# Kernel tuning notes

Measured on AMD Instinct MI355X. Metric: run time of the kernel, lower is better.

## Reference

```python
import jax, jax.numpy as jnp
import numpy as np
import math

D_MODEL = 1024
NUM_HEADS = 16
D_K = D_MODEL // NUM_HEADS


def setup_inputs() -> dict:
    key = jax.random.key(0)
    ks = jax.random.split(key, 9)
    s = 1.0 / math.sqrt(D_MODEL)
    x = jax.random.normal(ks[0], (2, 2048, D_MODEL), dtype=jnp.float32)
    # torch Linear params: weight [out, in], bias [out]
    Wq = jax.random.uniform(ks[1], (D_MODEL, D_MODEL), jnp.float32, -s, s)
    bq = jax.random.uniform(ks[2], (D_MODEL,), jnp.float32, -s, s)
    Wk = jax.random.uniform(ks[3], (D_MODEL, D_MODEL), jnp.float32, -s, s)
    bk = jax.random.uniform(ks[4], (D_MODEL,), jnp.float32, -s, s)
    Wv = jax.random.uniform(ks[5], (D_MODEL, D_MODEL), jnp.float32, -s, s)
    bv = jax.random.uniform(ks[6], (D_MODEL,), jnp.float32, -s, s)
    Wo = jax.random.uniform(ks[7], (D_MODEL, D_MODEL), jnp.float32, -s, s)
    bo = jax.random.uniform(ks[8], (D_MODEL,), jnp.float32, -s, s)
    return {"x": x, "Wq": Wq, "bq": bq, "Wk": Wk, "bk": bk,
            "Wv": Wv, "bv": bv, "Wo": Wo, "bo": bo}


def reference(x, Wq, bq, Wk, bk, Wv, bv, Wo, bo):
    B, T, _ = x.shape
    scale = 1.0 / math.sqrt(D_MODEL)  # NOTE: module scales by sqrt(d_model), not sqrt(d_k)

    def proj(W, b):
        # torch Linear: x @ W^T + b, then split heads -> [B, H, T, d_k]
        y = jnp.einsum('btd,ed->bte', x, W) + b
        return y.reshape(B, T, NUM_HEADS, D_K).transpose(0, 2, 1, 3)

    Q = proj(Wq, bq)
    K = proj(Wk, bk)
    V = proj(Wv, bv)
    logits = jnp.einsum('bhtd,bhsd->bhts', Q, K) * scale  # [B,H,T,T]
    attn = jax.nn.softmax(logits, axis=-1)
    out = jnp.einsum('bhts,bhsd->bhtd', attn, V)  # [B,H,T,d_k]
    out = out.transpose(0, 2, 1, 3).reshape(B, T, D_MODEL)
    return jnp.einsum('btd,ed->bte', out, Wo) + bo
```

## Files before the change

### kernel.cpp

```cpp
#include <hip/hip_runtime.h>

#define T_SEQ 2048
#define NB 2
#define NH 16
#define DK 64
#define DMODEL 1024

typedef __bf16 bf16x8 __attribute__((ext_vector_type(8)));
typedef float f32x4 __attribute__((ext_vector_type(4)));
typedef unsigned short ushortx8 __attribute__((ext_vector_type(8)));
typedef unsigned short ushortx4 __attribute__((ext_vector_type(4)));

__device__ inline unsigned short f2b1(float f) {
  unsigned u = __float_as_uint(f);
  u += 0x7fffu + ((u >> 16) & 1u);
  return (unsigned short)(u >> 16);
}

__device__ inline void gload16(const void* g, void* l) {
  __builtin_amdgcn_global_load_lds((const __attribute__((address_space(1))) void*)g,
                                   (__attribute__((address_space(3))) void*)l, 16, 0, 0);
}

__device__ inline bf16x8 mk8(unsigned a, unsigned b, unsigned c, unsigned d) {
  uint4 t = {a, b, c, d};
  return *(bf16x8*)&t;
}

__device__ inline unsigned cvtpk(float lo, float hi) {
  unsigned r;
  asm("v_cvt_pk_bf16_f32 %0, %1, %2" : "=v"(r) : "v"(lo), "v"(hi));
  return r;
}

__global__ void prep(const float* __restrict__ x,
                     const float* __restrict__ w0, const float* __restrict__ w1,
                     const float* __restrict__ w2, const float* __restrict__ w3,
                     const float* __restrict__ bq, const float* __restrict__ bk,
                     const float* __restrict__ bv,
                     unsigned short* __restrict__ xb, unsigned short* __restrict__ Wqkv,
                     float* __restrict__ bqkv) {
  int bid = blockIdx.x, tid = threadIdx.x;
  if (bid < 4096) {
    int i = (bid * 256 + tid) * 4;
    float4 v = *(const float4*)(x + i);
    ushortx4 o;
    o.x = f2b1(v.x); o.y = f2b1(v.y); o.z = f2b1(v.z); o.w = f2b1(v.w);
    *(ushortx4*)(xb + i) = o;
  } else if (bid < 8192) {
    int which = (bid - 4096) >> 10;
    int i = (((bid - 4096) & 1023) * 256 + tid) * 4;
    const float* src = which == 0 ? w0 : which == 1 ? w1 : which == 2 ? w2 : w3;
    float4 v = *(const float4*)(src + i);
    ushortx4 o;
    o.x = f2b1(v.x); o.y = f2b1(v.y); o.z = f2b1(v.z); o.w = f2b1(v.w);
    *(ushortx4*)(Wqkv + (long)which * 1048576 + i) = o;
  } else {
    int i = (bid - 8192) * 256 + tid;
    if (i < 3072) {
      float v = (i < 1024) ? bq[i] : (i < 2048 ? bk[i - 1024] : bv[i - 2048]);
      bqkv[i] = v;
    }
  }
}

__global__ __launch_bounds__(256, 3)
void gemm_qkv(const unsigned short* __restrict__ A, const unsigned short* __restrict__ B,
              const float* __restrict__ bias, unsigned short* __restrict__ Cb,
              unsigned short* __restrict__ Vt, int M, int N, int K, float scl) {
  __shared__ unsigned short As[2][4096];
  __shared__ unsigned short Bs[2][4096];
  const int tid = threadIdx.x;
  const int w = tid >> 6, lane = tid & 63;
  const int quad = lane >> 4, l16 = lane & 15;
  const int bm = blockIdx.y, bn = blockIdx.x;
  const int wm = w >> 1, wn = w & 1;

  f32x4 acc[4][4] = {};

  const int srow = tid >> 2;
  const int c4 = tid & 3;
  const unsigned short* aG = A + (long)(bm * 128 + srow) * K + c4 * 8;
  const unsigned short* bG = B + (long)(bn * 128 + srow) * K + c4 * 8;
  const long rs64 = (long)64 * K;
  const int wo = w * 512;

  gload16(aG, As[0] + wo);
  gload16(aG + rs64, As[0] + 2048 + wo);
  gload16(bG, Bs[0] + wo);
  gload16(bG + rs64, Bs[0] + 2048 + wo);

  int buf = 0;
  for (int kt = 0; kt < K; kt += 32) {
    __syncthreads();
    {
      const int nb = buf ^ 1;
      gload16(aG + kt + 32, As[nb] + wo);
      gload16(aG + rs64 + kt + 32, As[nb] + 2048 + wo);
      gload16(bG + kt + 32, Bs[nb] + wo);
      gload16(bG + rs64 + kt + 32, Bs[nb] + 2048 + wo);
    }

    bf16x8 af[4], bfr[4];
#pragma unroll
    for (int mt = 0; mt < 4; mt++)
      af[mt] = *(const bf16x8*)(As[buf] + (wm * 64 + mt * 16 + l16) * 32 + quad * 8);
#pragma unroll
    for (int nt = 0; nt < 4; nt++)
      bfr[nt] = *(const bf16x8*)(Bs[buf] + (wn * 64 + nt * 16 + l16) * 32 + quad * 8);
#pragma unroll
    for (int mt = 0; mt < 4; mt++)
#pragma unroll
      for (int nt = 0; nt < 4; nt++)
        acc[mt][nt] = __builtin_amdgcn_mfma_f32_16x16x32_bf16(af[mt], bfr[nt], acc[mt][nt], 0, 0, 0);
    buf ^= 1;
  }

  const int col0 = bn * 128 + wn * 64 + l16;
  const bool isV = (bn * 128) >= 2048;
#pragma unroll
  for (int mt = 0; mt < 4; mt++) {
    int row0 = bm * 128 + wm * 64 + mt * 16 + quad * 4;
#pragma unroll
    for (int nt = 0; nt < 4; nt++) {
      int col = col0 + nt * 16;
      float bb = bias[col];
      float s = (col < 1024) ? scl : 1.0f;
      if (!isV) {
#pragma unroll
        for (int r = 0; r < 4; r++)
          Cb[(long)(row0 + r) * N + col] = f2b1((acc[mt][nt][r] + bb) * s);
      } else {
        int cv = col - 2048;
        int h = cv >> 6, d = cv & 63;
        int b = row0 >> 11, t0 = row0 & 2047;
        int a = (t0 & 31) >> 2;
        int t0p = (t0 & ~31) | ((a & 3) << 3) | ((a >> 2) << 2);
        ushortx4 o;
        o.x = f2b1(acc[mt][nt][0] + bb);
        o.y = f2b1(acc[mt][nt][1] + bb);
        o.z = f2b1(acc[mt][nt][2] + bb);
        o.w = f2b1(acc[mt][nt][3] + bb);
        *(ushortx4*)(Vt + ((long)((b * NH + h) * DK + d)) * T_SEQ + t0p) = o;
      }
    }
  }
}

__global__ __launch_bounds__(256, 2)
void gemm_out(const unsigned short* __restrict__ A, const unsigned short* __restrict__ B,
              const float* __restrict__ bias, float* __restrict__ Cf, int M, int N, int K) {
  __shared__ unsigned short As[2][2048];
  __shared__ unsigned short Bs[2][4096];
  const int tid = threadIdx.x;
  const int w = tid >> 6, lane = tid & 63;
  const int quad = lane >> 4, l16 = lane & 15;
  const int bm = blockIdx.y, bn = blockIdx.x;
  const int wm = w >> 1, wn = w & 1;

  f32x4 acc[2][4] = {};

  const int srow = tid >> 2;
  const int c4 = tid & 3;
  const unsigned short* aG = A + (long)(bm * 64 + srow) * K + c4 * 8;
  const unsigned short* bG = B + (long)(bn * 128 + srow) * K + c4 * 8;
  const long rs64 = (long)64 * K;
  const int wo = w * 512;

  gload16(aG, As[0] + wo);
  gload16(bG, Bs[0] + wo);
  gload16(bG + rs64, Bs[0] + 2048 + wo);

  int buf = 0;
  for (int kt = 0; kt < K; kt += 32) {
    __syncthreads();
    {
      const int nb = buf ^ 1;
      gload16(aG + kt + 32, As[nb] + wo);
      gload16(bG + kt + 32, Bs[nb] + wo);
      gload16(bG + rs64 + kt + 32, Bs[nb] + 2048 + wo);
    }

    bf16x8 af[2], bfr[4];
#pragma unroll
    for (int mt = 0; mt < 2; mt++)
      af[mt] = *(const bf16x8*)(As[buf] + (wm * 32 + mt * 16 + l16) * 32 + quad * 8);
#pragma unroll
    for (int nt = 0; nt < 4; nt++)
      bfr[nt] = *(const bf16x8*)(Bs[buf] + (wn * 64 + nt * 16 + l16) * 32 + quad * 8);
#pragma unroll
    for (int mt = 0; mt < 2; mt++)
#pragma unroll
      for (int nt = 0; nt < 4; nt++)
        acc[mt][nt] = __builtin_amdgcn_mfma_f32_16x16x32_bf16(af[mt], bfr[nt], acc[mt][nt], 0, 0, 0);
    buf ^= 1;
  }

  const int col0 = bn * 128 + wn * 64 + l16;
#pragma unroll
  for (int mt = 0; mt < 2; mt++) {
    int row0 = bm * 64 + wm * 32 + mt * 16 + quad * 4;
#pragma unroll
    for (int nt = 0; nt < 4; nt++) {
      int col = col0 + nt * 16;
      float bb = bias[col];
#pragma unroll
      for (int r = 0; r < 4; r++)
        Cf[(long)(row0 + r) * N + col] = acc[mt][nt][r] + bb;
    }
  }
}

__global__ __launch_bounds__(256, 2)
void attn3(const unsigned short* __restrict__ QKV, const unsigned short* __restrict__ Vt,
           unsigned short* __restrict__ Ob) {
  __shared__ unsigned short Ks[2][4096];
  __shared__ unsigned short Vs[2][4096];
  const int tid = threadIdx.x;
  const int w = tid >> 6, lane = tid & 63;
  const int quad = lane >> 4, l16 = lane & 15;

  const int id = blockIdx.x;
  const int bh = id & 31;
  const int qt = id >> 5;
  const int b = bh >> 4, h = bh & 15;
  const long qkvBase = (long)b * T_SEQ * 3072;

  bf16x8 qf[2][2];
#pragma unroll
  for (int g = 0; g < 2; g++) {
    const unsigned short* qp = QKV + qkvBase + (long)(qt * 128 + w * 32 + g * 16 + l16) * 3072 + h * 64 + quad * 8;
    qf[g][0] = *(const bf16x8*)qp;
    qf[g][1] = *(const bf16x8*)(qp + 32);
  }

  const unsigned short* kG[2];
  const unsigned short* vG[2];
#pragma unroll
  for (int i = 0; i < 2; i++) {
    int S = w * 128 + i * 64 + lane;
    int row = S >> 3;
    int c = (S & 7) ^ (row & 7);
    kG[i] = QKV + qkvBase + 1024 + h * 64 + (long)row * 3072 + c * 8;
    vG[i] = Vt + (long)bh * DK * T_SEQ + (long)row * T_SEQ + c * 8;
  }
  const int wo2 = w * 1024;

  gload16(kG[0], Ks[0] + wo2);
  gload16(kG[1], Ks[0] + wo2 + 512);
  gload16(vG[0], Vs[0] + wo2);
  gload16(vG[1], Vs[0] + wo2 + 512);
  kG[0] += 64 * 3072; kG[1] += 64 * 3072;
  vG[0] += 64;        vG[1] += 64;

  const unsigned onesu = 0x3F803F80u;
  const bf16x8 ones = mk8(onesu, onesu, onesu, onesu);

  f32x4 acco[2][4] = {};
  f32x4 accp[2] = {};
  int buf = 0;
  const int e16 = (l16 & 7) * 16;

  for (int it = 0; it < 32; it++) {
    __syncthreads();
    if (it < 31) {
      const int nb = buf ^ 1;
      gload16(kG[0], Ks[nb] + wo2);
      gload16(kG[1], Ks[nb] + wo2 + 512);
      gload16(vG[0], Vs[nb] + wo2);
      gload16(vG[1], Vs[nb] + wo2 + 512);
      kG[0] += 64 * 3072; kG[1] += 64 * 3072;
      vG[0] += 64;        vG[1] += 64;
    }

    f32x4 st[2][4];
    __builtin_amdgcn_s_setprio(1);
#pragma unroll
    for (int nt = 0; nt < 4; nt++) {
      const char* kr = (char*)(Ks[buf]) + (nt * 16 + l16) * 128;
      bf16x8 k0 = *(const bf16x8*)(kr + ((quad * 16) ^ e16));
      bf16x8 k1 = *(const bf16x8*)(kr + (((quad + 4) * 16) ^ e16));
#pragma unroll
      for (int g = 0; g < 2; g++) {
        f32x4 z = {};
        z = __builtin_amdgcn_mfma_f32_16x16x32_bf16(k0, qf[g][0], z, 0, 0, 0);
        z = __builtin_amdgcn_mfma_f32_16x16x32_bf16(k1, qf[g][1], z, 0, 0, 0);
        st[g][nt] = z;
      }
    }
    __builtin_amdgcn_s_setprio(0);

    bf16x8 pa[2][2];
#pragma unroll
    for (int g = 0; g < 2; g++) {
      unsigned pk[4][2];
#pragma unroll
      for (int nt = 0; nt < 4; nt++) {
        float p0 = __builtin_amdgcn_exp2f(st[g][nt][0]);
        float p1 = __builtin_amdgcn_exp2f(st[g][nt][1]);
        float p2 = __builtin_amdgcn_exp2f(st[g][nt][2]);
        float p3 = __builtin_amdgcn_exp2f(st[g][nt][3]);
        pk[nt][0] = cvtpk(p0, p1);
        pk[nt][1] = cvtpk(p2, p3);
      }
      pa[g][0] = mk8(pk[0][0], pk[0][1], pk[1][0], pk[1][1]);
      pa[g][1] = mk8(pk[2][0], pk[2][1], pk[3][0], pk[3][1]);
      accp[g] = __builtin_amdgcn_mfma_f32_16x16x32_bf16(pa[g][0], ones, accp[g], 0, 0, 0);
      accp[g] = __builtin_amdgcn_mfma_f32_16x16x32_bf16(pa[g][1], ones, accp[g], 0, 0, 0);
    }

    __builtin_amdgcn_s_setprio(1);
#pragma unroll
    for (int nt = 0; nt < 4; nt++) {
      const char* vr = (char*)(Vs[buf]) + (nt * 16 + l16) * 128;
#pragma unroll
      for (int km = 0; km < 2; km++) {
        bf16x8 vf = *(const bf16x8*)(vr + (((km * 4 + quad) * 16) ^ e16));
#pragma unroll
        for (int g = 0; g < 2; g++)
          acco[g][nt] = __builtin_amdgcn_mfma_f32_16x16x32_bf16(pa[g][km], vf, acco[g][nt], 0, 0, 0);
      }
    }
    __builtin_amdgcn_s_setprio(0);
    buf ^= 1;
  }

  const int t0 = qt * 128 + w * 32;
#pragma unroll
  for (int g = 0; g < 2; g++) {
    f32x4 rl;
#pragma unroll
    for (int r = 0; r < 4; r++) rl[r] = __builtin_amdgcn_rcpf(accp[g][r]);
#pragma unroll
    for (int nt = 0; nt < 4; nt++)
#pragma unroll
      for (int r = 0; r < 4; r++) {
        int t = t0 + g * 16 + quad * 4 + r;
        Ob[(long)(b * T_SEQ + t) * DMODEL + h * 64 + nt * 16 + l16] = f2b1(acco[g][nt][r] * rl[r]);
      }
  }
}

extern "C" void kernel_launch(void* const* d_in, const int* in_sizes, int n_in,
                              void* d_out, int out_size, void* d_ws, size_t ws_size,
                              hipStream_t stream) {
  const float* x  = (const float*)d_in[0];
  const float* Wq = (const float*)d_in[1];
  const float* bq = (const float*)d_in[2];
  const float* Wk = (const float*)d_in[3];
  const float* bk = (const float*)d_in[4];
  const float* Wv = (const float*)d_in[5];
  const float* bv = (const float*)d_in[6];
  const float* Wo = (const float*)d_in[7];
  const float* bo = (const float*)d_in[8];
  float* out = (float*)d_out;

  unsigned short* xb   = (unsigned short*)d_ws;
  unsigned short* Wqkv = xb + 4194304;
  unsigned short* Wob  = Wqkv + 3145728;
  float*          bqkv = (float*)(Wob + 1048576);
  unsigned short* QKV  = (unsigned short*)(bqkv + 3072);
  unsigned short* Vt   = QKV + 12582912;
  unsigned short* Ob   = Vt + 4194304;

  prep<<<8204, 256, 0, stream>>>(x, Wq, Wk, Wv, Wo, bq, bk, bv, xb, Wqkv, bqkv);

  gemm_qkv<<<dim3(24, 32), 256, 0, stream>>>(xb, Wqkv, bqkv, QKV, Vt,
                                             4096, 3072, 1024, 0.04508422037f);

  attn3<<<dim3(512), 256, 0, stream>>>(QKV, Vt, Ob);

  gemm_out<<<dim3(8, 64), 256, 0, stream>>>(Ob, Wob, bo, out, 4096, 1024, 1024);
}
```

Baseline: 186.0 us.

## Software-pipeline attention loop to overlap exp softmax with next QK MFMAs

Restructures the attention main loop into a software pipeline. Each iteration now computes the exponentials for the previous tile's scores while issuing the QK^T MFMAs for the current tile, and V fragments are preloaded into registers for the next PV step. The loop is unrolled by two with ping-pong score buffers, plus a prologue and epilogue. The aim is to hide the transcendental and conversion latency behind matrix work, at the cost of higher register pressure, which could hurt occupancy at 2 blocks per SIMD.

```diff
diff --git a/kernel.cpp b/kernel.cpp
--- a/kernel.cpp
+++ b/kernel.cpp
@@ -211,6 +211,72 @@
   }
 }
 
+
+#define ATTN_BODY(IT, STP, STC)                                               \
+  {                                                                           \
+    const int cur = (IT) & 1;                                                 \
+    __syncthreads();                                                          \
+    if ((IT) < 31) {                                                          \
+      const int nb = cur ^ 1;                                                 \
+      gload16(kG[0], Ks[nb] + wo2);                                           \
+      gload16(kG[1], Ks[nb] + wo2 + 512);                                     \
+      gload16(vG[0], Vs[nb] + wo2);                                           \
+      gload16(vG[1], Vs[nb] + wo2 + 512);                                     \
+      kG[0] += 64 * 3072; kG[1] += 64 * 3072;                                 \
+      vG[0] += 64;        vG[1] += 64;                                        \
+    }                                                                         \
+    bf16x8 pa[2][2];                                                          \
+    _Pragma("unroll")                                                         \
+    for (int g = 0; g < 2; g++) {                                             \
+      unsigned pk[4][2];                                                      \
+      _Pragma("unroll")                                                       \
+      for (int nt = 0; nt < 4; nt++) {                                        \
+        float p0 = __builtin_amdgcn_exp2f(STP[g][nt][0]);                     \
+        float p1 = __builtin_amdgcn_exp2f(STP[g][nt][1]);                     \
+        float p2 = __builtin_amdgcn_exp2f(STP[g][nt][2]);                     \
+        float p3 = __builtin_amdgcn_exp2f(STP[g][nt][3]);                     \
+        pk[nt][0] = cvtpk(p0, p1);                                            \
+        pk[nt][1] = cvtpk(p2, p3);                                            \
+      }                                                                       \
+      pa[g][0] = mk8(pk[0][0], pk[0][1], pk[1][0], pk[1][1]);                 \
+      pa[g][1] = mk8(pk[2][0], pk[2][1], pk[3][0], pk[3][1]);                 \
+    }                                                                         \
+    __builtin_amdgcn_s_setprio(1);                                            \
+    _Pragma("unroll")                                                         \
+    for (int nt = 0; nt < 4; nt++) {                                          \
+      const char* kr = (char*)(Ks[cur]) + (nt * 16 + l16) * 128;              \
+      bf16x8 k0 = *(const bf16x8*)(kr + ((quad * 16) ^ e16));                 \
+      bf16x8 k1 = *(const bf16x8*)(kr + (((quad + 4) * 16) ^ e16));           \
+      _Pragma("unroll")                                                       \
+      for (int g = 0; g < 2; g++) {                                           \
+        f32x4 z = {};                                                         \
+        z = __builtin_amdgcn_mfma_f32_16x16x32_bf16(k0, qf[g][0], z, 0, 0, 0);\
+        z = __builtin_amdgcn_mfma_f32_16x16x32_bf16(k1, qf[g][1], z, 0, 0, 0);\
+        STC[g][nt] = z;                                                       \
+      }                                                                       \
+    }                                                                         \
+    _Pragma("unroll")                                                         \
+    for (int g = 0; g < 2; g++) {                                             \
+      accp[g] = __builtin_amdgcn_mfma_f32_16x16x32_bf16(pa[g][0], ones, accp[g], 0, 0, 0); \
+      accp[g] = __builtin_amdgcn_mfma_f32_16x16x32_bf16(pa[g][1], ones, accp[g], 0, 0, 0); \
+    }                                                                         \
+    _Pragma("unroll")                                                         \
+    for (int nt = 0; nt < 4; nt++)                                            \
+      _Pragma("unroll")                                                       \
+      for (int km = 0; km < 2; km++)                                          \
+        _Pragma("unroll")                                                     \
+        for (int g = 0; g < 2; g++)                                           \
+          acco[g][nt] = __builtin_amdgcn_mfma_f32_16x16x32_bf16(pa[g][km], vreg[nt][km], acco[g][nt], 0, 0, 0); \
+    __builtin_amdgcn_s_setprio(0);                                            \
+    _Pragma("unroll")                                                         \
+    for (int nt = 0; nt < 4; nt++) {                                          \
+      const char* vr = (char*)(Vs[cur]) + (nt * 16 + l16) * 128;              \
+      _Pragma("unroll")                                                       \
+      for (int km = 0; km < 2; km++)                                          \
+        vreg[nt][km] = *(const bf16x8*)(vr + (((km * 4 + quad) * 16) ^ e16)); \
+    }                                                                         \
+  }
+
 __global__ __launch_bounds__(256, 2)
 void attn3(const unsigned short* __restrict__ QKV, const unsigned short* __restrict__ Vt,
            unsigned short* __restrict__ Ob) {
@@ -246,60 +312,67 @@
   }
   const int wo2 = w * 1024;
 
+  const unsigned onesu = 0x3F803F80u;
+  const bf16x8 ones = mk8(onesu, onesu, onesu, onesu);
+
+  f32x4 acco[2][4] = {};
+  f32x4 accp[2] = {};
+  bf16x8 vreg[4][2];
+  f32x4 stA[2][4], stB[2][4];
+  const int e16 = (l16 & 7) * 16;
+
   gload16(kG[0], Ks[0] + wo2);
   gload16(kG[1], Ks[0] + wo2 + 512);
   gload16(vG[0], Vs[0] + wo2);
   gload16(vG[1], Vs[0] + wo2 + 512);
   kG[0] += 64 * 3072; kG[1] += 64 * 3072;
   vG[0] += 64;        vG[1] += 64;
-
-  const unsigned onesu = 0x3F803F80u;
-  const bf16x8 ones = mk8(onesu, onesu, onesu, onesu);
-
-  f32x4 acco[2][4] = {};
-  f32x4 accp[2] = {};
-  int buf = 0;
-  const int e16 = (l16 & 7) * 16;
-
-  for (int it = 0; it < 32; it++) {
-    __syncthreads();
-    if (it < 31) {
-      const int nb = buf ^ 1;
-      gload16(kG[0], Ks[nb] + wo2);
-      gload16(kG[1], Ks[nb] + wo2 + 512);
-      gload16(vG[0], Vs[nb] + wo2);
-      gload16(vG[1], Vs[nb] + wo2 + 512);
-      kG[0] += 64 * 3072; kG[1] += 64 * 3072;
-      vG[0] += 64;        vG[1] += 64;
-    }
-
-    f32x4 st[2][4];
-    __builtin_amdgcn_s_setprio(1);
-#pragma unroll
-    for (int nt = 0; nt < 4; nt++) {
-      const char* kr = (char*)(Ks[buf]) + (nt * 16 + l16) * 128;
-      bf16x8 k0 = *(const bf16x8*)(kr + ((quad * 16) ^ e16));
-      bf16x8 k1 = *(const bf16x8*)(kr + (((quad + 4) * 16) ^ e16));
-#pragma unroll
-      for (int g = 0; g < 2; g++) {
-        f32x4 z = {};
-        z = __builtin_amdgcn_mfma_f32_16x16x32_bf16(k0, qf[g][0], z, 0, 0, 0);
-        z = __builtin_amdgcn_mfma_f32_16x16x32_bf16(k1, qf[g][1], z, 0, 0, 0);
-        st[g][nt] = z;
-      }
-    }
-    __builtin_amdgcn_s_setprio(0);
-
+  __syncthreads();
+  gload16(kG[0], Ks[1] + wo2);
+  gload16(kG[1], Ks[1] + wo2 + 512);
+  gload16(vG[0], Vs[1] + wo2);
+  gload16(vG[1], Vs[1] + wo2 + 512);
+  kG[0] += 64 * 3072; kG[1] += 64 * 3072;
+  vG[0] += 64;        vG[1] += 64;
+#pragma unroll
+  for (int nt = 0; nt < 4; nt++) {
+    const char* kr = (char*)(Ks[0]) + (nt * 16 + l16) * 128;
+    bf16x8 k0 = *(const bf16x8*)(kr + ((quad * 16) ^ e16));
+    bf16x8 k1 = *(const bf16x8*)(kr + (((quad + 4) * 16) ^ e16));
+#pragma unroll
+    for (int g = 0; g < 2; g++) {
+      f32x4 z = {};
+      z = __builtin_amdgcn_mfma_f32_16x16x32_bf16(k0, qf[g][0], z, 0, 0, 0);
+      z = __builtin_amdgcn_mfma_f32_16x16x32_bf16(k1, qf[g][1], z, 0, 0, 0);
+      stA[g][nt] = z;
+    }
+  }
+#pragma unroll
+  for (int nt = 0; nt < 4; nt++) {
+    const char* vr = (char*)(Vs[0]) + (nt * 16 + l16) * 128;
+#pragma unroll
+    for (int km = 0; km < 2; km++)
+      vreg[nt][km] = *(const bf16x8*)(vr + (((km * 4 + quad) * 16) ^ e16));
+  }
+
+#pragma unroll 1
+  for (int it = 1; it < 31; it += 2) {
+    ATTN_BODY(it, stA, stB);
+    ATTN_BODY(it + 1, stB, stA);
+  }
+  ATTN_BODY(31, stA, stB);
+
+  {
     bf16x8 pa[2][2];
 #pragma unroll
     for (int g = 0; g < 2; g++) {
       unsigned pk[4][2];
 #pragma unroll
       for (int nt = 0; nt < 4; nt++) {
-        float p0 = __builtin_amdgcn_exp2f(st[g][nt][0]);
-        float p1 = __builtin_amdgcn_exp2f(st[g][nt][1]);
-        float p2 = __builtin_amdgcn_exp2f(st[g][nt][2]);
-        float p3 = __builtin_amdgcn_exp2f(st[g][nt][3]);
+        float p0 = __builtin_amdgcn_exp2f(stB[g][nt][0]);
+        float p1 = __builtin_amdgcn_exp2f(stB[g][nt][1]);
+        float p2 = __builtin_amdgcn_exp2f(stB[g][nt][2]);
+        float p3 = __builtin_amdgcn_exp2f(stB[g][nt][3]);
         pk[nt][0] = cvtpk(p0, p1);
         pk[nt][1] = cvtpk(p2, p3);
       }
@@ -308,21 +381,13 @@
       accp[g] = __builtin_amdgcn_mfma_f32_16x16x32_bf16(pa[g][0], ones, accp[g], 0, 0, 0);
       accp[g] = __builtin_amdgcn_mfma_f32_16x16x32_bf16(pa[g][1], ones, accp[g], 0, 0, 0);
     }
-
-    __builtin_amdgcn_s_setprio(1);
-#pragma unroll
-    for (int nt = 0; nt < 4; nt++) {
-      const char* vr = (char*)(Vs[buf]) + (nt * 16 + l16) * 128;
-#pragma unroll
-      for (int km = 0; km < 2; km++) {
-        bf16x8 vf = *(const bf16x8*)(vr + (((km * 4 + quad) * 16) ^ e16));
+#pragma unroll
+    for (int nt = 0; nt < 4; nt++)
+#pragma unroll
+      for (int km = 0; km < 2; km++)
 #pragma unroll
         for (int g = 0; g < 2; g++)
-          acco[g][nt] = __builtin_amdgcn_mfma_f32_16x16x32_bf16(pa[g][km], vf, acco[g][nt], 0, 0, 0);
-      }
-    }
-    __builtin_amdgcn_s_setprio(0);
-    buf ^= 1;
+          acco[g][nt] = __builtin_amdgcn_mfma_f32_16x16x32_bf16(pa[g][km], vreg[nt][km], acco[g][nt], 0, 0, 0);
   }
 
   const int t0 = qt * 128 + w * 32;
```

New measurement: 178.0 us, median of 3. 1.04x faster.
